# Optimization experiments

Measured on AMD Instinct MI355X. Metric: run time of the kernel, lower is better.

The kernel has to match this reference:

```python
import jax, jax.numpy as jnp
import numpy as np
from jax import lax

B, S, E, CC, H, NH, K = 8, 2048, 128, 256, 256, 8, 7
HD = H // NH  # head dim = 32


def setup_inputs() -> dict:
    key = jax.random.key(0)
    ks = jax.random.split(key, 16)
    x = jax.random.normal(ks[0], (B, S, E), dtype=jnp.float32)
    lengths = jax.random.randint(ks[1], (B,), S // 2, S + 1)
    mask = (jnp.arange(S)[None, :] < lengths[:, None])  # contiguous prefix padding mask
    sc = 0.02
    return {
        "x": x,
        "mask": mask,
        "conv_w": jax.random.normal(ks[2], (CC, E, K), dtype=jnp.float32) * sc,
        "conv_b": jnp.zeros((CC,), jnp.float32),
        "wq": jax.random.normal(ks[3], (CC, H), dtype=jnp.float32) * sc,
        "bq": jnp.zeros((H,), jnp.float32),
        "wk": jax.random.normal(ks[4], (CC, H), dtype=jnp.float32) * sc,
        "bk": jnp.zeros((H,), jnp.float32),
        "wv": jax.random.normal(ks[5], (CC, H), dtype=jnp.float32) * sc,
        "bv": jnp.zeros((H,), jnp.float32),
        "fc_w": jax.random.normal(ks[6], (H, CC), dtype=jnp.float32) * sc,
        "fc_b": jnp.zeros((CC,), jnp.float32),
        "ln_g": jnp.ones((CC,), jnp.float32),
        "ln_b": jnp.zeros((CC,), jnp.float32),
        "gamma": jnp.float32(0.5),
        "std_param": jnp.float32(0.2),
    }


def _penalty(mask, gamma, std_param):
    # (B, S, S) Gaussian penalty, nonzero only in the valid_len x valid_len block
    valid_len = mask.sum(axis=-1).astype(jnp.float32)  # (B,)
    idx = jnp.arange(S, dtype=jnp.float32)
    valid = (jnp.arange(S)[None, :] < mask.sum(axis=-1)[:, None]).astype(jnp.float32)  # (B,S)
    norm_pos = (idx[None, :] + 1.0) / (valid_len[:, None] + 1.0)  # (B,S)
    std = jnp.clip(std_param, 0.01, 0.5)
    base = jnp.exp(-((norm_pos - 0.5) ** 2) / (2.0 * std * std))
    pvec = base * (jnp.exp(gamma) - 1.0) * valid  # (B,S)
    pen = 0.5 * (pvec[:, :, None] + pvec[:, None, :])
    return pen * valid[:, :, None] * valid[:, None, :]


def reference(x, mask, conv_w, conv_b, wq, bq, wk, bk, wv, bv, fc_w, fc_b, ln_g, ln_b, gamma, std_param):
    # Conv1d frontend: (B,S,E) -> (B,E,S) -> conv -> relu -> (B,S,CC)
    xt = jnp.transpose(x, (0, 2, 1))
    y = lax.conv_general_dilated(xt, conv_w, window_strides=(1,), padding=[(K // 2, K // 2)])
    y = jax.nn.relu(y + conv_b[None, :, None])
    h = jnp.transpose(y, (0, 2, 1))  # (B,S,CC)

    q = (h @ wq + bq).reshape(B, S, NH, HD).transpose(0, 2, 1, 3)
    k = (h @ wk + bk).reshape(B, S, NH, HD).transpose(0, 2, 1, 3)
    v = (h @ wv + bv).reshape(B, S, NH, HD).transpose(0, 2, 1, 3)

    scores = jnp.einsum('bnqd,bnkd->bnqk', q, k) / np.sqrt(HD).astype(np.float32)
    scores = scores - _penalty(mask, gamma, std_param)[:, None, :, :]
    scores = jnp.where(mask[:, None, None, :], scores, jnp.float32(-1e10))
    probs = jax.nn.softmax(scores, axis=-1)
    ctx = jnp.einsum('bnqk,bnkd->bnqd', probs, v)
    ctx = ctx.transpose(0, 2, 1, 3).reshape(B, S, H)
    out = ctx @ fc_w + fc_b

    z = h + out
    mu = z.mean(-1, keepdims=True)
    var = ((z - mu) ** 2).mean(-1, keepdims=True)
    return (z - mu) / jnp.sqrt(var + 1e-5) * ln_g + ln_b
```

## Files before the change

kernel.cpp:

```cpp
#include <hip/hip_runtime.h>
#include <hip/hip_bf16.h>

#define B_ 8
#define S_ 2048
#define E_ 128
#define CC_ 256
#define H_ 256
#define NH_ 8
#define HD_ 32
#define KW_ 7

typedef __attribute__((ext_vector_type(8))) short bf16x8;
typedef __attribute__((ext_vector_type(4))) float f32x4;
typedef __attribute__((ext_vector_type(16))) float f32x16;

#define QSCALE_ (0.17677669529663687f * 1.4426950408889634f)
#define CPEN_   0.7213475204444817f

static __device__ __forceinline__ unsigned short f2bf(float f) {
    __hip_bfloat16 h = __float2bfloat16(f);
    return *(unsigned short*)&h;
}
static __device__ __forceinline__ float bf2f(unsigned short u) {
    __hip_bfloat16 h = *(__hip_bfloat16*)&u;
    return __bfloat162float(h);
}
static __device__ __forceinline__ void perm32swap(unsigned& a, unsigned& b) {
    asm volatile("s_nop 1\n\tv_permlane32_swap_b32 %0, %1" : "+v"(a), "+v"(b));
}

__global__ __launch_bounds__(256) void prep_kernel(
    const float* __restrict__ cw, const float* __restrict__ wq,
    const float* __restrict__ wk, const float* __restrict__ wv,
    const float* __restrict__ fw, const void* __restrict__ mask,
    const float* __restrict__ gamma_p, const float* __restrict__ std_p,
    unsigned short* __restrict__ wre2, unsigned short* __restrict__ wqkv2,
    unsigned short* __restrict__ wf2, float* __restrict__ ctab,
    int* __restrict__ lenv)
{
    __shared__ int cnt[256];
    const int blk = blockIdx.x, tid = threadIdx.x;

    if (blk < 896) {
        int i = blk * 256 + tid;
        int kl = i & 31, cc = (i >> 5) & 255, eb = (i >> 13) & 3, kk = i >> 15;
        wre2[i] = f2bf(cw[cc * (E_ * KW_) + (eb * 32 + kl) * KW_ + kk]);
    } else if (blk < 1664) {
        int i = (blk - 896) * 256 + tid;
        int kl = i & 31, col = (i >> 5) & 255, kb = (i >> 13) & 7, m = i >> 16;
        const float* W = (m == 0) ? wq : (m == 1) ? wk : wv;
        wqkv2[i] = f2bf(W[(kb * 32 + kl) * H_ + col]);
    } else if (blk < 1920) {
        int i = (blk - 1664) * 256 + tid;
        int kl = i & 31, col = (i >> 5) & 255, kb = i >> 13;
        wf2[i] = f2bf(fw[(kb * 32 + kl) * CC_ + col]);
    } else {
        int b = blk - 1920;

        uint32_t w0 = ((const uint32_t*)mask)[0];
        int mode = 0;
        if (w0 == 0x01010101u) mode = 1;
        else if (w0 == 0x3F803F80u) mode = 2;
        else if (w0 == 0x3F800000u) mode = 3;

        int c = 0;
        for (int s = tid; s < S_; s += 256) {
            bool vv;
            size_t i = (size_t)b * S_ + s;
            if (mode == 0)      vv = ((const int*)mask)[i] != 0;
            else if (mode == 1) vv = ((const unsigned char*)mask)[i] != 0;
            else if (mode == 2) vv = (((const unsigned short*)mask)[i] & 0x7FFFu) != 0;
            else                vv = ((const float*)mask)[i] != 0.f;
            c += vv ? 1 : 0;
        }
        cnt[tid] = c;
        __syncthreads();
        for (int off = 128; off > 0; off >>= 1) {
            if (tid < off) cnt[tid] += cnt[tid + off];
            __syncthreads();
        }
        int L = cnt[0];
        if (tid == 0) lenv[b] = L;

        float Lf = (float)L;
        float gamma = gamma_p[0];
        float sd = std_p[0];
        sd = fminf(fmaxf(sd, 0.01f), 0.5f);
        float scale = expf(gamma) - 1.f;
        float inv2s2 = 1.f / (2.f * sd * sd);
        float* row0 = ctab + (size_t)b * 2 * S_;
        float* row1 = row0 + S_;
        for (int s = tid; s < S_; s += 256) {
            float np = (s + 1.f) / (Lf + 1.f);
            float e = np - 0.5f;
            float base = expf(-(e * e) * inv2s2);
            bool vkk = s < L;
            row0[s] = vkk ? 0.f : -1e10f;
            row1[s] = vkk ? (-CPEN_ * base * scale) : -1e10f;
        }
    }
}

__global__ __launch_bounds__(256) void front_kernel(
    const float* __restrict__ x, const unsigned short* __restrict__ wre2,
    const float* __restrict__ cb, const unsigned short* __restrict__ wqkv2,
    const float* __restrict__ bq, const float* __restrict__ bk,
    const float* __restrict__ bv, unsigned short* __restrict__ hb,
    unsigned short* __restrict__ qo, unsigned short* __restrict__ ko,
    unsigned short* __restrict__ vo)
{
    __shared__ __align__(16) char smem[64 * 264 * 2];
    short (*xl)[136] = (short(*)[136])smem;
    short (*Al)[264] = (short(*)[264])smem;

    const int tid = threadIdx.x, wave = tid >> 6, lane = tid & 63;
    const int l15 = lane & 15, l4 = lane >> 4;
    const int s0 = blockIdx.x * 64, b = blockIdx.y;

    for (int idx = tid; idx < 70 * 32; idx += 256) {
        int row = idx >> 5, c4 = idx & 31;
        int pos = s0 - 3 + row;
        float4 v = {0.f, 0.f, 0.f, 0.f};
        if (pos >= 0 && pos < S_)
            v = *(const float4*)(x + ((size_t)b * S_ + pos) * E_ + c4 * 4);
        short* p = &xl[row][c4 * 4];
        p[0] = (short)f2bf(v.x); p[1] = (short)f2bf(v.y);
        p[2] = (short)f2bf(v.z); p[3] = (short)f2bf(v.w);
    }
    __syncthreads();

    f32x4 acc[4][4];
#pragma unroll
    for (int i = 0; i < 4; i++)
#pragma unroll
        for (int j = 0; j < 4; j++) acc[i][j] = (f32x4){0.f, 0.f, 0.f, 0.f};

#pragma unroll 1
    for (int kk = 0; kk < KW_; kk++) {
#pragma unroll
        for (int eb = 0; eb < 4; eb++) {
            const unsigned short* wp =
                wre2 + (((size_t)(kk * 4 + eb) * 256 + wave * 64 + l15) * 32) + l4 * 8;
            bf16x8 af[4], bfr[4];
#pragma unroll
            for (int ct = 0; ct < 4; ct++)
                bfr[ct] = *(const bf16x8*)(wp + ct * 512);
#pragma unroll
            for (int rt = 0; rt < 4; rt++)
                af[rt] = *(const bf16x8*)(&xl[rt * 16 + l15 + kk][eb * 32 + l4 * 8]);
#pragma unroll
            for (int rt = 0; rt < 4; rt++)
#pragma unroll
                for (int ct = 0; ct < 4; ct++)
                    acc[rt][ct] = __builtin_amdgcn_mfma_f32_16x16x32_bf16(
                        af[rt], bfr[ct], acc[rt][ct], 0, 0, 0);
        }
    }
    __syncthreads();

#pragma unroll
    for (int ct = 0; ct < 4; ct++) {
        int col = wave * 64 + ct * 16 + l15;
        float bias = cb[col];
#pragma unroll
        for (int rt = 0; rt < 4; rt++)
#pragma unroll
            for (int r = 0; r < 4; r++) {
                float v0 = acc[rt][ct][r] + bias;
                v0 = v0 > 0.f ? v0 : 0.f;
                Al[rt * 16 + l4 * 4 + r][col] = (short)f2bf(v0);
            }
    }
    __syncthreads();

    for (int idx = tid; idx < 64 * 32; idx += 256) {
        int row = idx >> 5, c8 = idx & 31;
        *(bf16x8*)(hb + ((size_t)b * S_ + s0 + row) * CC_ + c8 * 8) =
            *(const bf16x8*)(&Al[row][c8 * 8]);
    }

#pragma unroll 1
    for (int m = 0; m < 3; m++) {
        f32x4 qacc[4][4];
#pragma unroll
        for (int i = 0; i < 4; i++)
#pragma unroll
            for (int j = 0; j < 4; j++) qacc[i][j] = (f32x4){0.f, 0.f, 0.f, 0.f};

#pragma unroll 1
        for (int kb8 = 0; kb8 < 8; kb8++) {
            const unsigned short* wp =
                wqkv2 + (((size_t)(m * 8 + kb8) * 256 + wave * 64 + l15) * 32) + l4 * 8;
            bf16x8 af[4], bfr[4];
#pragma unroll
            for (int ct = 0; ct < 4; ct++)
                bfr[ct] = *(const bf16x8*)(wp + ct * 512);
#pragma unroll
            for (int rt = 0; rt < 4; rt++)
                af[rt] = *(const bf16x8*)(&Al[rt * 16 + l15][kb8 * 32 + l4 * 8]);
#pragma unroll
            for (int rt = 0; rt < 4; rt++)
#pragma unroll
                for (int ct = 0; ct < 4; ct++)
                    qacc[rt][ct] = __builtin_amdgcn_mfma_f32_16x16x32_bf16(
                        af[rt], bfr[ct], qacc[rt][ct], 0, 0, 0);
        }

        const float* bias_p = (m == 0) ? bq : (m == 1) ? bk : bv;
        unsigned short* O = (m == 0) ? qo : (m == 1) ? ko : vo;
        const float oscale = (m == 0) ? QSCALE_ : 1.f;
#pragma unroll
        for (int ct = 0; ct < 4; ct++) {
            int col = wave * 64 + ct * 16 + l15;
            float bias = bias_p[col];
            int n = col >> 5, d = col & 31;
#pragma unroll
            for (int rt = 0; rt < 4; rt++)
#pragma unroll
                for (int r = 0; r < 4; r++) {
                    int row = s0 + rt * 16 + l4 * 4 + r;
                    O[(((size_t)b * NH_ + n) * S_ + row) * HD_ + d] =
                        f2bf((qacc[rt][ct][r] + bias) * oscale);
                }
        }
    }
}

__global__ __launch_bounds__(256) void attn_mfma_kernel(
    const unsigned short* __restrict__ q, const unsigned short* __restrict__ k,
    const unsigned short* __restrict__ v, const float* __restrict__ ctab,
    const int* __restrict__ lenv, unsigned short* __restrict__ ctxb)
{
    __shared__ short Kt[2][128][40];
    __shared__ short Vt[2][32][136];
    __shared__ __align__(16) float ctC[2][2][128];

    const int tid = threadIdx.x;
    const int wave = tid >> 6, lane = tid & 63;
    const int r31 = lane & 31, hi = lane >> 5;
    const int hi8 = hi * 8, hi4 = hi * 4;

    const int qt = blockIdx.x, n = blockIdx.y, b = blockIdx.z;
    const int qrow = qt * 128 + wave * 32 + r31;
    const int L = lenv[b];
    const int nt = (L + 127) >> 7;

    const size_t head = ((size_t)b * NH_ + n) * S_;
    const unsigned short* qbase = q + head * HD_;
    const unsigned short* kbase = k + head * HD_;
    const unsigned short* vbase = v + head * HD_;
    const float* ct0 = ctab + (size_t)b * 2 * S_;
    const float* ct1 = ct0 + S_;

    bf16x8 qf0 = *(const bf16x8*)(qbase + (size_t)qrow * HD_ + hi8);
    bf16x8 qf1 = *(const bf16x8*)(qbase + (size_t)qrow * HD_ + 16 + hi8);
    const int crow = (qrow < L) ? 1 : 0;

    bf16x8 ones;
#pragma unroll
    for (int i = 0; i < 8; i++) ones[i] = (short)0x3F80;

    f32x16 acc, acc_l;
#pragma unroll
    for (int r = 0; r < 16; r++) { acc[r] = 0.f; acc_l[r] = 0.f; }
    float m_r = 0.f;

    const int krow = tid >> 1, kch = (tid & 1) * 16;
    const int d7x2 = 2 * (r31 & 7);
    const int vc = krow >> 3, vk7 = krow & 7;

    bf16x8 kreg0, kreg1, va, vb;
    float c0r = 0.f, c1r = 0.f;

    kreg0 = *(const bf16x8*)(kbase + (size_t)krow * HD_ + kch);
    kreg1 = *(const bf16x8*)(kbase + (size_t)krow * HD_ + kch + 8);
    va    = *(const bf16x8*)(vbase + (size_t)krow * HD_ + kch);
    vb    = *(const bf16x8*)(vbase + (size_t)krow * HD_ + kch + 8);
    if (tid < 128) { c0r = ct0[tid]; c1r = ct1[tid]; }
    {
        *(bf16x8*)(&Kt[0][krow][kch])     = kreg0;
        *(bf16x8*)(&Kt[0][krow][kch + 8]) = kreg1;
#pragma unroll
        for (int i = 0; i < 8; i++) {
            int d0 = kch + i, d1 = kch + 8 + i;
            Vt[0][d0][((((vc - 2 * (d0 & 7)) & 7) | (vc & 8)) << 3) + vk7] = va[i];
            Vt[0][d1][((((vc - 2 * (d1 & 7)) & 7) | (vc & 8)) << 3) + vk7] = vb[i];
        }
        if (tid < 128) { ctC[0][0][tid] = c0r; ctC[0][1][tid] = c1r; }
    }
    __syncthreads();

#pragma unroll 1
    for (int t = 0; t < nt; t++) {
        const int cur = t & 1;
        const int knext = (t + 1) << 7;
        const bool more = (t + 1 < nt);

        if (more) {
            kreg0 = *(const bf16x8*)(kbase + (size_t)(knext + krow) * HD_ + kch);
            kreg1 = *(const bf16x8*)(kbase + (size_t)(knext + krow) * HD_ + kch + 8);
            va    = *(const bf16x8*)(vbase + (size_t)(knext + krow) * HD_ + kch);
            vb    = *(const bf16x8*)(vbase + (size_t)(knext + krow) * HD_ + kch + 8);
            if (tid < 128) { c0r = ct0[knext + tid]; c1r = ct1[knext + tid]; }
        }

        __builtin_amdgcn_s_setprio(1);
        f32x16 sc[4];
        if (__all(m_r == 0.f)) {
#pragma unroll
            for (int t4 = 0; t4 < 4; t4++) {
                bf16x8 kf0 = *(const bf16x8*)(&Kt[cur][t4 * 32 + r31][hi8]);
                bf16x8 kf1 = *(const bf16x8*)(&Kt[cur][t4 * 32 + r31][16 + hi8]);
                f32x16 c0;
#pragma unroll
                for (int g = 0; g < 4; g++) {
                    f32x4 cp = *(const f32x4*)(&ctC[cur][crow][t4 * 32 + g * 8 + hi4]);
#pragma unroll
                    for (int j = 0; j < 4; j++) c0[g * 4 + j] = cp[j];
                }
                f32x16 s1 = __builtin_amdgcn_mfma_f32_32x32x16_bf16(kf0, qf0, c0, 0, 0, 0);
                sc[t4] = __builtin_amdgcn_mfma_f32_32x32x16_bf16(kf1, qf1, s1, 0, 0, 0);
            }
        } else {
#pragma unroll
            for (int t4 = 0; t4 < 4; t4++) {
                bf16x8 kf0 = *(const bf16x8*)(&Kt[cur][t4 * 32 + r31][hi8]);
                bf16x8 kf1 = *(const bf16x8*)(&Kt[cur][t4 * 32 + r31][16 + hi8]);
                f32x16 c0;
#pragma unroll
                for (int g = 0; g < 4; g++) {
                    f32x4 cp = *(const f32x4*)(&ctC[cur][crow][t4 * 32 + g * 8 + hi4]);
#pragma unroll
                    for (int j = 0; j < 4; j++) c0[g * 4 + j] = cp[j] - m_r;
                }
                f32x16 s1 = __builtin_amdgcn_mfma_f32_32x32x16_bf16(kf0, qf0, c0, 0, 0, 0);
                sc[t4] = __builtin_amdgcn_mfma_f32_32x32x16_bf16(kf1, qf1, s1, 0, 0, 0);
            }
        }
        __builtin_amdgcn_s_setprio(0);

        float mxa[4];
#pragma unroll
        for (int g = 0; g < 4; g++) mxa[g] = -1e30f;
#pragma unroll
        for (int t4 = 0; t4 < 4; t4++)
#pragma unroll
            for (int g = 0; g < 4; g++)
                mxa[g] = fmaxf(fmaxf(fmaxf(mxa[g], sc[t4][g * 4]),
                                     fmaxf(sc[t4][g * 4 + 1], sc[t4][g * 4 + 2])),
                               sc[t4][g * 4 + 3]);
        float pmx = fmaxf(fmaxf(mxa[0], mxa[1]), fmaxf(mxa[2], mxa[3]));

        if (!__all(pmx <= 8.f)) {
            pmx = fmaxf(pmx, __shfl_xor(pmx, 32, 64));
            float d = fmaxf(pmx, 0.f);
            float alpha = exp2f(-d);
            m_r += d;
#pragma unroll
            for (int t4 = 0; t4 < 4; t4++)
#pragma unroll
                for (int r = 0; r < 16; r++) sc[t4][r] -= d;
#pragma unroll
            for (int r = 0; r < 16; r++) acc[r] *= alpha;
            acc_l[0] *= alpha;
        }

        unsigned pk[4][8];
#pragma unroll
        for (int t4 = 0; t4 < 4; t4++) {
            unsigned U[8];
#pragma unroll
            for (int j = 0; j < 8; j++) {
                float pa = exp2f(sc[t4][2 * j]);
                float pb = exp2f(sc[t4][2 * j + 1]);
                U[j] = (unsigned)f2bf(pa) | ((unsigned)f2bf(pb) << 16);
            }
            perm32swap(U[0], U[2]);
            perm32swap(U[1], U[3]);
            perm32swap(U[4], U[6]);
            perm32swap(U[5], U[7]);
            pk[t4][0] = U[0]; pk[t4][1] = U[1]; pk[t4][2] = U[2]; pk[t4][3] = U[3];
            pk[t4][4] = U[4]; pk[t4][5] = U[5]; pk[t4][6] = U[6]; pk[t4][7] = U[7];
        }

        __builtin_amdgcn_s_setprio(1);
#pragma unroll
        for (int t4 = 0; t4 < 4; t4++) {
            union { unsigned u[4]; bf16x8 v8; } pb0, pb1;
            pb0.u[0] = pk[t4][0]; pb0.u[1] = pk[t4][1];
            pb0.u[2] = pk[t4][2]; pb0.u[3] = pk[t4][3];
            pb1.u[0] = pk[t4][4]; pb1.u[1] = pk[t4][5];
            pb1.u[2] = pk[t4][6]; pb1.u[3] = pk[t4][7];
            int c0i = t4 * 4 + hi, c1i = t4 * 4 + 2 + hi;
            bf16x8 vf0 = *(const bf16x8*)(&Vt[cur][r31][(((c0i - d7x2) & 7) | (c0i & 8)) << 3]);
            bf16x8 vf1 = *(const bf16x8*)(&Vt[cur][r31][(((c1i - d7x2) & 7) | (c1i & 8)) << 3]);
            acc   = __builtin_amdgcn_mfma_f32_32x32x16_bf16(vf0, pb0.v8, acc, 0, 0, 0);
            acc_l = __builtin_amdgcn_mfma_f32_32x32x16_bf16(ones, pb0.v8, acc_l, 0, 0, 0);
            acc   = __builtin_amdgcn_mfma_f32_32x32x16_bf16(vf1, pb1.v8, acc, 0, 0, 0);
            acc_l = __builtin_amdgcn_mfma_f32_32x32x16_bf16(ones, pb1.v8, acc_l, 0, 0, 0);
        }
        __builtin_amdgcn_s_setprio(0);

        if (more) {
            const int nxt = cur ^ 1;
            *(bf16x8*)(&Kt[nxt][krow][kch])     = kreg0;
            *(bf16x8*)(&Kt[nxt][krow][kch + 8]) = kreg1;
#pragma unroll
            for (int i = 0; i < 8; i++) {
                int d0 = kch + i, d1 = kch + 8 + i;
                Vt[nxt][d0][((((vc - 2 * (d0 & 7)) & 7) | (vc & 8)) << 3) + vk7] = va[i];
                Vt[nxt][d1][((((vc - 2 * (d1 & 7)) & 7) | (vc & 8)) << 3) + vk7] = vb[i];
            }
            if (tid < 128) { ctC[nxt][0][tid] = c0r; ctC[nxt][1][tid] = c1r; }
            __syncthreads();
        }
    }

    float inv = 1.f / acc_l[0];
    size_t obase = ((size_t)b * S_ + qrow) * H_ + n * HD_;
#pragma unroll
    for (int g = 0; g < 4; g++)
#pragma unroll
        for (int w = 0; w < 2; w++) {
            unsigned uo = (unsigned)f2bf(acc[g * 4 + w * 2] * inv) |
                          ((unsigned)f2bf(acc[g * 4 + w * 2 + 1] * inv) << 16);
            int d = 8 * g + hi4 + 2 * w;
            *(unsigned*)(ctxb + obase + d) = uo;
        }
}

__global__ __launch_bounds__(256) void fc_ln_mfma_kernel(
    const unsigned short* __restrict__ ctxb, const unsigned short* __restrict__ hb,
    const unsigned short* __restrict__ wf2, const float* __restrict__ fb,
    const float* __restrict__ g, const float* __restrict__ bbias,
    float* __restrict__ out)
{
    const int tid = threadIdx.x, wave = tid >> 6, lane = tid & 63;
    const int l15 = lane & 15, l4 = lane >> 4;
    const int s0 = blockIdx.x * 64, b = blockIdx.y;
    const int arow = s0 + wave * 16 + l15;

    bf16x8 af[8];
#pragma unroll
    for (int kb = 0; kb < 8; kb++)
        af[kb] = *(const bf16x8*)(ctxb + (size_t)((size_t)b * S_ + arow) * H_ + kb * 32 + l4 * 8);

    f32x4 acc[16];
#pragma unroll
    for (int ct = 0; ct < 16; ct++) acc[ct] = (f32x4){0.f, 0.f, 0.f, 0.f};

#pragma unroll 1
    for (int kb = 0; kb < 8; kb++) {
        const unsigned short* wp = wf2 + ((size_t)kb * 256 + l15) * 32 + l4 * 8;
#pragma unroll
        for (int ct = 0; ct < 16; ct++) {
            bf16x8 bfr = *(const bf16x8*)(wp + ct * 512);
            acc[ct] = __builtin_amdgcn_mfma_f32_16x16x32_bf16(af[kb], bfr, acc[ct], 0, 0, 0);
        }
    }

    float fbias[16];
#pragma unroll
    for (int ct = 0; ct < 16; ct++) fbias[ct] = fb[ct * 16 + l15];

#pragma unroll
    for (int r = 0; r < 4; r++) {
        int row = s0 + wave * 16 + l4 * 4 + r;
        size_t ro = ((size_t)b * S_ + row) * CC_;
        float z[16];
        float sum = 0.f;
#pragma unroll
        for (int ct = 0; ct < 16; ct++) {
            float zz = acc[ct][r] + fbias[ct] + bf2f(hb[ro + ct * 16 + l15]);
            z[ct] = zz;
            sum += zz;
        }
#pragma unroll
        for (int off = 1; off < 16; off <<= 1) sum += __shfl_xor(sum, off, 64);
        float mu = sum * (1.f / 256.f);
        float vs = 0.f;
#pragma unroll
        for (int ct = 0; ct < 16; ct++) {
            float d = z[ct] - mu;
            z[ct] = d;
            vs += d * d;
        }
#pragma unroll
        for (int off = 1; off < 16; off <<= 1) vs += __shfl_xor(vs, off, 64);
        float inv = rsqrtf(vs * (1.f / 256.f) + 1e-5f);
#pragma unroll
        for (int ct = 0; ct < 16; ct++) {
            int col = ct * 16 + l15;
            out[ro + col] = z[ct] * inv * g[col] + bbias[col];
        }
    }
}

extern "C" void kernel_launch(void* const* d_in, const int* in_sizes, int n_in,
                              void* d_out, int out_size, void* d_ws, size_t ws_size,
                              hipStream_t stream)
{
    const float* x      = (const float*)d_in[0];
    const void*  mask   = d_in[1];
    const float* conv_w = (const float*)d_in[2];
    const float* conv_b = (const float*)d_in[3];
    const float* wq     = (const float*)d_in[4];
    const float* bq     = (const float*)d_in[5];
    const float* wk     = (const float*)d_in[6];
    const float* bk     = (const float*)d_in[7];
    const float* wv     = (const float*)d_in[8];
    const float* bv     = (const float*)d_in[9];
    const float* fc_w   = (const float*)d_in[10];
    const float* fc_b   = (const float*)d_in[11];
    const float* ln_g   = (const float*)d_in[12];
    const float* ln_b   = (const float*)d_in[13];
    const float* gamma  = (const float*)d_in[14];
    const float* stdp   = (const float*)d_in[15];

    char* ws = (char*)d_ws;
    const size_t MB = 1024 * 1024;
    unsigned short* hb    = (unsigned short*)(ws);
    unsigned short* qb    = (unsigned short*)(ws + 8 * MB);
    unsigned short* kb    = (unsigned short*)(ws + 16 * MB);
    unsigned short* vb    = (unsigned short*)(ws + 24 * MB);
    unsigned short* ctxb  = (unsigned short*)(ws + 32 * MB);
    float*          ctab  = (float*)(ws + 40 * MB);
    int*            lenv  = (int*)(ws + 40 * MB + 256 * 1024);
    unsigned short* wre2  = (unsigned short*)(ws + 41 * MB);
    unsigned short* wqkv2 = (unsigned short*)(ws + 42 * MB);
    unsigned short* wf2   = (unsigned short*)(ws + 43 * MB);

    prep_kernel<<<1928, 256, 0, stream>>>(conv_w, wq, wk, wv, fc_w, mask,
                                          gamma, stdp, wre2, wqkv2, wf2,
                                          ctab, lenv);
    dim3 g2(S_ / 64, B_);
    front_kernel<<<g2, 256, 0, stream>>>(x, wre2, conv_b, wqkv2, bq, bk, bv,
                                         hb, qb, kb, vb);
    dim3 ag(S_ / 128, NH_, B_);
    attn_mfma_kernel<<<ag, 256, 0, stream>>>(qb, kb, vb, ctab, lenv, ctxb);
    fc_ln_mfma_kernel<<<g2, 256, 0, stream>>>(ctxb, hb, wf2, fc_b, ln_g, ln_b,
                                              (float*)d_out);
}
```

Baseline: 188.0 us.

## Fold key penalty and mask bias into an extra bf16 MFMA K-step

The per-key penalty and mask bias are packed as two bf16 values in the K tile's padding columns. They are applied through a third MFMA against a per-row selector vector in q, which replaces the fp32 ctab shared-memory loads used to seed the accumulator. The online-softmax max handling is restructured so the running max is subtracted after the score MFMAs, not preloaded into the accumulator. This adds one MFMA per tile and rounds the penalty to bf16, trading a little precision and extra matrix work for fewer LDS reads and VALU ops.

New measurement: 186.5 us. Within noise of the previous version (-0.8%).

```diff
diff --git a/kernel.cpp b/kernel.cpp
--- a/kernel.cpp
+++ b/kernel.cpp
@@ -35,7 +35,7 @@
     const float* __restrict__ fw, const void* __restrict__ mask,
     const float* __restrict__ gamma_p, const float* __restrict__ std_p,
     unsigned short* __restrict__ wre2, unsigned short* __restrict__ wqkv2,
-    unsigned short* __restrict__ wf2, float* __restrict__ ctab,
+    unsigned short* __restrict__ wf2, unsigned* __restrict__ ctp,
     int* __restrict__ lenv)
 {
     __shared__ int cnt[256];
@@ -88,15 +88,15 @@
         sd = fminf(fmaxf(sd, 0.01f), 0.5f);
         float scale = expf(gamma) - 1.f;
         float inv2s2 = 1.f / (2.f * sd * sd);
-        float* row0 = ctab + (size_t)b * 2 * S_;
-        float* row1 = row0 + S_;
+        unsigned* row = ctp + (size_t)b * S_;
         for (int s = tid; s < S_; s += 256) {
             float np = (s + 1.f) / (Lf + 1.f);
             float e = np - 0.5f;
             float base = expf(-(e * e) * inv2s2);
             bool vkk = s < L;
-            row0[s] = vkk ? 0.f : -1e10f;
-            row1[s] = vkk ? (-CPEN_ * base * scale) : -1e10f;
+            unsigned short pen_h = vkk ? f2bf(-CPEN_ * base * scale) : (unsigned short)0;
+            unsigned short msk_h = vkk ? (unsigned short)0 : f2bf(-1e10f);
+            row[s] = (unsigned)pen_h | ((unsigned)msk_h << 16);
         }
     }
 }
@@ -228,12 +228,11 @@
 
 __global__ __launch_bounds__(256) void attn_mfma_kernel(
     const unsigned short* __restrict__ q, const unsigned short* __restrict__ k,
-    const unsigned short* __restrict__ v, const float* __restrict__ ctab,
+    const unsigned short* __restrict__ v, const unsigned* __restrict__ ctp,
     const int* __restrict__ lenv, unsigned short* __restrict__ ctxb)
 {
     __shared__ short Kt[2][128][40];
     __shared__ short Vt[2][32][136];
-    __shared__ __align__(16) float ctC[2][2][128];
 
     const int tid = threadIdx.x;
     const int wave = tid >> 6, lane = tid & 63;
@@ -249,16 +248,25 @@
     const unsigned short* qbase = q + head * HD_;
     const unsigned short* kbase = k + head * HD_;
     const unsigned short* vbase = v + head * HD_;
-    const float* ct0 = ctab + (size_t)b * 2 * S_;
-    const float* ct1 = ct0 + S_;
+    const unsigned* ctpb = ctp + (size_t)b * S_;
 
     bf16x8 qf0 = *(const bf16x8*)(qbase + (size_t)qrow * HD_ + hi8);
     bf16x8 qf1 = *(const bf16x8*)(qbase + (size_t)qrow * HD_ + 16 + hi8);
-    const int crow = (qrow < L) ? 1 : 0;
+
+    bf16x8 qe;
+#pragma unroll
+    for (int i = 0; i < 8; i++) qe[i] = 0;
+    if (hi == 0) {
+        qe[0] = (qrow < L) ? (short)0x3F80 : (short)0;
+        qe[1] = (short)0x3F80;
+    }
 
     bf16x8 ones;
 #pragma unroll
     for (int i = 0; i < 8; i++) ones[i] = (short)0x3F80;
+    f32x16 zc;
+#pragma unroll
+    for (int r = 0; r < 16; r++) zc[r] = 0.f;
 
     f32x16 acc, acc_l;
 #pragma unroll
@@ -270,14 +278,18 @@
     const int vc = krow >> 3, vk7 = krow & 7;
 
     bf16x8 kreg0, kreg1, va, vb;
-    float c0r = 0.f, c1r = 0.f;
+    unsigned cw = 0;
 
     kreg0 = *(const bf16x8*)(kbase + (size_t)krow * HD_ + kch);
     kreg1 = *(const bf16x8*)(kbase + (size_t)krow * HD_ + kch + 8);
     va    = *(const bf16x8*)(vbase + (size_t)krow * HD_ + kch);
     vb    = *(const bf16x8*)(vbase + (size_t)krow * HD_ + kch + 8);
-    if (tid < 128) { c0r = ct0[tid]; c1r = ct1[tid]; }
+    if (tid < 128) cw = ctpb[tid];
     {
+        short* pr = &Kt[tid >> 7][tid & 127][34];
+        *(unsigned*)(pr) = 0; *(unsigned*)(pr + 2) = 0; *(unsigned*)(pr + 4) = 0;
+        if (tid < 4) *(unsigned*)(&Kt[1][0][tid * 2]) = 0;
+
         *(bf16x8*)(&Kt[0][krow][kch])     = kreg0;
         *(bf16x8*)(&Kt[0][krow][kch + 8]) = kreg1;
 #pragma unroll
@@ -286,7 +298,7 @@
             Vt[0][d0][((((vc - 2 * (d0 & 7)) & 7) | (vc & 8)) << 3) + vk7] = va[i];
             Vt[0][d1][((((vc - 2 * (d1 & 7)) & 7) | (vc & 8)) << 3) + vk7] = vb[i];
         }
-        if (tid < 128) { ctC[0][0][tid] = c0r; ctC[0][1][tid] = c1r; }
+        if (tid < 128) *(unsigned*)(&Kt[0][tid][32]) = cw;
     }
     __syncthreads();
 
@@ -301,41 +313,20 @@
             kreg1 = *(const bf16x8*)(kbase + (size_t)(knext + krow) * HD_ + kch + 8);
             va    = *(const bf16x8*)(vbase + (size_t)(knext + krow) * HD_ + kch);
             vb    = *(const bf16x8*)(vbase + (size_t)(knext + krow) * HD_ + kch + 8);
-            if (tid < 128) { c0r = ct0[knext + tid]; c1r = ct1[knext + tid]; }
+            if (tid < 128) cw = ctpb[knext + tid];
         }
 
         __builtin_amdgcn_s_setprio(1);
         f32x16 sc[4];
-        if (__all(m_r == 0.f)) {
-#pragma unroll
-            for (int t4 = 0; t4 < 4; t4++) {
-                bf16x8 kf0 = *(const bf16x8*)(&Kt[cur][t4 * 32 + r31][hi8]);
-                bf16x8 kf1 = *(const bf16x8*)(&Kt[cur][t4 * 32 + r31][16 + hi8]);
-                f32x16 c0;
-#pragma unroll
-                for (int g = 0; g < 4; g++) {
-                    f32x4 cp = *(const f32x4*)(&ctC[cur][crow][t4 * 32 + g * 8 + hi4]);
-#pragma unroll
-                    for (int j = 0; j < 4; j++) c0[g * 4 + j] = cp[j];
-                }
-                f32x16 s1 = __builtin_amdgcn_mfma_f32_32x32x16_bf16(kf0, qf0, c0, 0, 0, 0);
-                sc[t4] = __builtin_amdgcn_mfma_f32_32x32x16_bf16(kf1, qf1, s1, 0, 0, 0);
-            }
-        } else {
-#pragma unroll
-            for (int t4 = 0; t4 < 4; t4++) {
-                bf16x8 kf0 = *(const bf16x8*)(&Kt[cur][t4 * 32 + r31][hi8]);
-                bf16x8 kf1 = *(const bf16x8*)(&Kt[cur][t4 * 32 + r31][16 + hi8]);
-                f32x16 c0;
-#pragma unroll
-                for (int g = 0; g < 4; g++) {
-                    f32x4 cp = *(const f32x4*)(&ctC[cur][crow][t4 * 32 + g * 8 + hi4]);
-#pragma unroll
-                    for (int j = 0; j < 4; j++) c0[g * 4 + j] = cp[j] - m_r;
-                }
-                f32x16 s1 = __builtin_amdgcn_mfma_f32_32x32x16_bf16(kf0, qf0, c0, 0, 0, 0);
-                sc[t4] = __builtin_amdgcn_mfma_f32_32x32x16_bf16(kf1, qf1, s1, 0, 0, 0);
-            }
+#pragma unroll
+        for (int t4 = 0; t4 < 4; t4++) {
+            const short* kr = &Kt[cur][t4 * 32 + r31][0];
+            bf16x8 kf0 = *(const bf16x8*)(kr + hi8);
+            bf16x8 kf1 = *(const bf16x8*)(kr + 16 + hi8);
+            bf16x8 kf2 = *(const bf16x8*)(kr + 32 + hi8);
+            f32x16 s0 = __builtin_amdgcn_mfma_f32_32x32x16_bf16(kf0, qf0, zc, 0, 0, 0);
+            f32x16 s1 = __builtin_amdgcn_mfma_f32_32x32x16_bf16(kf1, qf1, s0, 0, 0, 0);
+            sc[t4]    = __builtin_amdgcn_mfma_f32_32x32x16_bf16(kf2, qe,  s1, 0, 0, 0);
         }
         __builtin_amdgcn_s_setprio(0);
 
@@ -351,18 +342,20 @@
                                sc[t4][g * 4 + 3]);
         float pmx = fmaxf(fmaxf(mxa[0], mxa[1]), fmaxf(mxa[2], mxa[3]));
 
-        if (!__all(pmx <= 8.f)) {
+        if (!__all(pmx <= m_r + 8.f)) {
             pmx = fmaxf(pmx, __shfl_xor(pmx, 32, 64));
-            float d = fmaxf(pmx, 0.f);
-            float alpha = exp2f(-d);
-            m_r += d;
-#pragma unroll
-            for (int t4 = 0; t4 < 4; t4++)
-#pragma unroll
-                for (int r = 0; r < 16; r++) sc[t4][r] -= d;
+            float mn = fmaxf(m_r, pmx);
+            float alpha = exp2f(m_r - mn);
+            m_r = mn;
 #pragma unroll
             for (int r = 0; r < 16; r++) acc[r] *= alpha;
             acc_l[0] *= alpha;
+        }
+        if (__any(m_r != 0.f)) {
+#pragma unroll
+            for (int t4 = 0; t4 < 4; t4++)
+#pragma unroll
+                for (int r = 0; r < 16; r++) sc[t4][r] -= m_r;
         }
 
         unsigned pk[4][8];
@@ -411,7 +404,7 @@
                 Vt[nxt][d0][((((vc - 2 * (d0 & 7)) & 7) | (vc & 8)) << 3) + vk7] = va[i];
                 Vt[nxt][d1][((((vc - 2 * (d1 & 7)) & 7) | (vc & 8)) << 3) + vk7] = vb[i];
             }
-            if (tid < 128) { ctC[nxt][0][tid] = c0r; ctC[nxt][1][tid] = c1r; }
+            if (tid < 128) *(unsigned*)(&Kt[nxt][tid][32]) = cw;
             __syncthreads();
         }
     }
@@ -524,7 +517,7 @@
     unsigned short* kb    = (unsigned short*)(ws + 16 * MB);
     unsigned short* vb    = (unsigned short*)(ws + 24 * MB);
     unsigned short* ctxb  = (unsigned short*)(ws + 32 * MB);
-    float*          ctab  = (float*)(ws + 40 * MB);
+    unsigned*       ctp   = (unsigned*)(ws + 40 * MB);
     int*            lenv  = (int*)(ws + 40 * MB + 256 * 1024);
     unsigned short* wre2  = (unsigned short*)(ws + 41 * MB);
     unsigned short* wqkv2 = (unsigned short*)(ws + 42 * MB);
@@ -532,12 +525,12 @@
 
     prep_kernel<<<1928, 256, 0, stream>>>(conv_w, wq, wk, wv, fc_w, mask,
                                           gamma, stdp, wre2, wqkv2, wf2,
-                                          ctab, lenv);
+                                          ctp, lenv);
     dim3 g2(S_ / 64, B_);
     front_kernel<<<g2, 256, 0, stream>>>(x, wre2, conv_b, wqkv2, bq, bk, bv,
                                          hb, qb, kb, vb);
     dim3 ag(S_ / 128, NH_, B_);
-    attn_mfma_kernel<<<ag, 256, 0, stream>>>(qb, kb, vb, ctab, lenv, ctxb);
+    attn_mfma_kernel<<<ag, 256, 0, stream>>>(qb, kb, vb, ctp, lenv, ctxb);
     fc_ln_mfma_kernel<<<g2, 256, 0, stream>>>(ctxb, hb, wf2, fc_b, ln_g, ln_b,
                                               (float*)d_out);
 }
```
